# Performance work log

Hardware: AMD Instinct MI355X
Metric: run time of the kernel (lower is better)

## Reference

```python
import jax, jax.numpy as jnp
import numpy as np

B, C_IN, C_OUT, A, H, W = 32, 256, 512, 256, 64, 64


def setup_inputs() -> dict:
    key = jax.random.key(0)
    ks = jax.random.split(key, 8)
    s = 0.02
    return {
        "x": jax.random.normal(ks[0], (B, C_IN, H, W), dtype=jnp.float32),
        "g": jax.random.normal(ks[1], (B, C_OUT), dtype=jnp.float32),
        "Wg": jax.random.normal(ks[2], (A, C_OUT), dtype=jnp.float32) * s,
        "bg": jnp.full((A,), 0.1, dtype=jnp.float32),
        "Wx": jax.random.normal(ks[3], (A, C_IN), dtype=jnp.float32) * s,
        "bx": jnp.full((A,), 0.1, dtype=jnp.float32),
        "Wf": jax.random.normal(ks[4], (1, A), dtype=jnp.float32) * s,
        "bf": jnp.full((1,), 0.1, dtype=jnp.float32),
    }


def reference(x, g, Wg, bg, Wx, bx, Wf, bf):
    b, c, h, w = x.shape
    gg = g @ Wg.T + bg                                  # [B, A]
    xf = x.reshape(b, c, h * w)                          # [B, C, HW]
    # Linear_x applied per spatial position (batched instead of python loop)
    nx = jnp.einsum('bcn,ac->bna', xf, Wx) + bx          # [B, HW, A]
    nx = jax.nn.relu(gg[:, None, :] + nx)                # [B, HW, A]
    att = jnp.einsum('bna,a->bn', nx, Wf[0]) + bf[0]     # [B, HW]
    # min-subtract, sum-divide normalization
    att = att - jnp.min(att, axis=1, keepdims=True)
    att = att / jnp.sum(att, axis=1, keepdims=True)
    out = jnp.einsum('bcn,bn->bc', xf, att)              # weighted pooling [B, C]
    return out, att.reshape(b, h, w)
```

## Files before the change

kernel.cpp:

```cpp
#include <hip/hip_runtime.h>
#include <stdint.h>

#define B_   32
#define CIN  256
#define COUT 512
#define A_   256
#define HW_  4096
#define NT   64
#define TILES 8

typedef short  short8  __attribute__((ext_vector_type(8)));
typedef float  float4_ __attribute__((ext_vector_type(4)));

typedef const __attribute__((address_space(1))) unsigned int glb_uint;
typedef __attribute__((address_space(3))) unsigned int lds_uint;

__device__ __forceinline__ unsigned f2bf(float f) {
    unsigned u = __float_as_uint(f);
    u += 0x7FFFu + ((u >> 16) & 1u);
    return u >> 16;
}
__device__ __forceinline__ float bf2f(unsigned h) {
    return __uint_as_float(h << 16);
}

__device__ __forceinline__ void bar_lds() {
    __builtin_amdgcn_sched_barrier(0);
    asm volatile("s_waitcnt lgkmcnt(0)" ::: "memory");
    __builtin_amdgcn_s_barrier();
    __builtin_amdgcn_sched_barrier(0);
}

__global__ __launch_bounds__(256) void prep_kernel(
    const float* __restrict__ g, const float* __restrict__ Wg,
    const float* __restrict__ bg, const float* __restrict__ Wx,
    const float* __restrict__ bx,
    uint4* __restrict__ WxR, float* __restrict__ ggbx,
    float* __restrict__ P, float* __restrict__ T)
{
    int t = threadIdx.x;
    if (blockIdx.x >= 32) {
        int e = (blockIdx.x - 32) * 256 + t;
        int lane = e & 63, ai = (e >> 6) & 3, kk = (e >> 8) & 7, w = e >> 11;
        int a  = w * 64 + ai * 16 + (lane & 15);
        int kb = kk * 32 + (lane >> 4) * 8;
        const float4* s = (const float4*)(Wx + (size_t)a * 256 + kb);
        float4 u0 = s[0], u1 = s[1];
        uint4 pk;
        pk.x = f2bf(u0.x) | (f2bf(u0.y) << 16);
        pk.y = f2bf(u0.z) | (f2bf(u0.w) << 16);
        pk.z = f2bf(u1.x) | (f2bf(u1.y) << 16);
        pk.w = f2bf(u1.z) | (f2bf(u1.w) << 16);
        WxR[e] = pk;
        return;
    }
    int b = blockIdx.x;
    int i = b * 256 + t;
    P[i] = 0.f; T[i] = 0.f;

    __shared__ float gl[COUT];
    gl[t]       = g[b * COUT + t];
    gl[t + 256] = g[b * COUT + 256 + t];
    __syncthreads();

    float acc0 = bg[t] + bx[t], acc1 = 0.f;
    const float4* wr = (const float4*)(Wg + (size_t)t * COUT);
    #pragma unroll 8
    for (int co = 0; co < COUT / 4; co += 2) {
        float4 wv0 = wr[co],     gv0 = *(const float4*)&gl[co * 4];
        float4 wv1 = wr[co + 1], gv1 = *(const float4*)&gl[co * 4 + 4];
        acc0 += wv0.x * gv0.x + wv0.y * gv0.y + wv0.z * gv0.z + wv0.w * gv0.w;
        acc1 += wv1.x * gv1.x + wv1.y * gv1.y + wv1.z * gv1.z + wv1.w * gv1.w;
    }
    ggbx[b * 256 + t] = acc0 + acc1;
}

__global__ __launch_bounds__(512)
__attribute__((amdgpu_waves_per_eu(2, 2)))
void attn_main(
    const float* __restrict__ x, const char* __restrict__ WxR,
    const float* __restrict__ ggbx, const float* __restrict__ Wf,
    const float* __restrict__ bfs,
    float* __restrict__ P, float* __restrict__ T, float* __restrict__ raw)
{
    __shared__ float        rawb[CIN * NT];
    __shared__ unsigned int xT[2][NT * 128];
    __shared__ float att_part[8][NT];
    __shared__ float raw_l[NT];

    int bid = blockIdx.x;
    int b = bid >> 3, tg = bid & 7;
    int t = threadIdx.x, w = t >> 6, lane = t & 63;
    int quad = lane >> 4, l15 = lane & 15;
    int st = (tg + b) & 7;

    const float* xb = x + (size_t)b * CIN * HW_ + tg * (TILES * NT);

    auto STAGE = [&](int tile) {
        const float* gb = xb + (size_t)(w * 32 + (lane >> 4)) * HW_
                             + tile * NT + (lane & 15) * 4;
        #pragma unroll
        for (int j = 0; j < 8; j++) {
            __builtin_amdgcn_global_load_lds(
                (glb_uint*)(gb + (size_t)j * 4 * HW_),
                (lds_uint*)&rawb[(w * 8 + j) * 256], 16, 0, 0);
        }
    };

    short8 bfp[16];
    {
        const char* wsl = WxR + (w >> 1) * 32768 + (w & 1) * 2048 + lane * 16;
        #pragma unroll
        for (int kk = 0; kk < 8; kk++) {
            bfp[kk * 2]     = *(const short8*)(wsl + kk * 4096);
            bfp[kk * 2 + 1] = *(const short8*)(wsl + kk * 4096 + 1024);
        }
    }

    float4_ ga4[2], wf4[2];
    #pragma unroll
    for (int ai = 0; ai < 2; ai++) {
        int a0 = w * 32 + ai * 16 + quad * 4;
        ga4[ai] = *(const float4_*)&ggbx[b * 256 + a0];
        wf4[ai] = *(const float4_*)&Wf[a0];
    }

    float pp[4] = {0.f, 0.f, 0.f, 0.f};
    float tt[4] = {0.f, 0.f, 0.f, 0.f};
    int qpt   = (t & 63) >> 1;
    int half  = (t & 1) * 8;
    int nbase = w * 8;

    STAGE(st);

    #pragma unroll 1
    for (int ii = 0; ii < TILES; ii++) {
        int it = (ii + st) & 7;
        unsigned int* xc = xT[ii & 1];

        __syncthreads();

        {
            int n = lane;
            #pragma unroll
            for (int p = 0; p < 4; p++) {
                int q = w * 4 + p;
                const float* rb = &rawb[(q * 8) * 64 + n];
                uint4 pk;
                pk.x = f2bf(rb[0])   | (f2bf(rb[64])  << 16);
                pk.y = f2bf(rb[128]) | (f2bf(rb[192]) << 16);
                pk.z = f2bf(rb[256]) | (f2bf(rb[320]) << 16);
                pk.w = f2bf(rb[384]) | (f2bf(rb[448]) << 16);
                *(uint4*)&xc[n * 128 + ((q ^ (n & 31)) << 2)] = pk;
            }
        }
        __syncthreads();

        if (ii < TILES - 1)
            STAGE((ii + 1 + st) & 7);

        const unsigned int* xl = xc;
        float4_ acc[4][2];
        #pragma unroll
        for (int mi = 0; mi < 4; mi++) {
            acc[mi][0] = (float4_){0.f, 0.f, 0.f, 0.f};
            acc[mi][1] = (float4_){0.f, 0.f, 0.f, 0.f};
        }
        short8 afA[4], afB[4];
        auto LDA = [&](short8* af, int k0) {
            int qk = (k0 >> 3) + quad;
            #pragma unroll
            for (int mi = 0; mi < 4; mi++) {
                int n = mi * 16 + l15;
                af[mi] = *(const short8*)&xl[n * 128 + ((qk ^ (n & 31)) << 2)];
            }
        };
        auto MM = [&](short8* af, int ks) {
            #pragma unroll
            for (int mi = 0; mi < 4; mi++) {
                acc[mi][0] = __builtin_amdgcn_mfma_f32_16x16x32_bf16(
                    bfp[ks * 2],     af[mi], acc[mi][0], 0, 0, 0);
                acc[mi][1] = __builtin_amdgcn_mfma_f32_16x16x32_bf16(
                    bfp[ks * 2 + 1], af[mi], acc[mi][1], 0, 0, 0);
            }
        };

        LDA(afA, 0);   LDA(afB, 32);
        MM(afA, 0);    LDA(afA, 64);
        MM(afB, 1);    LDA(afB, 96);
        MM(afA, 2);    LDA(afA, 128);
        MM(afB, 3);    LDA(afB, 160);
        MM(afA, 4);    LDA(afA, 192);
        MM(afB, 5);    LDA(afB, 224);
        MM(afA, 6);
        MM(afB, 7);

        #pragma unroll
        for (int mi = 0; mi < 4; mi++) {
            float p = 0.f;
            #pragma unroll
            for (int ai = 0; ai < 2; ai++) {
                #pragma unroll
                for (int r = 0; r < 4; r++) {
                    float vv = fmaxf(acc[mi][ai][r] + ga4[ai][r], 0.f);
                    p = fmaf(vv, wf4[ai][r], p);
                }
            }
            p += __shfl_xor(p, 16, 64);
            p += __shfl_xor(p, 32, 64);
            if (quad == 0) att_part[w][mi * 16 + l15] = p;
        }
        bar_lds();

        if (t < NT) {
            float rv = att_part[0][t] + att_part[1][t] + att_part[2][t] + att_part[3][t]
                     + att_part[4][t] + att_part[5][t] + att_part[6][t] + att_part[7][t]
                     + bfs[0];
            raw[b * HW_ + (tg * TILES + it) * NT + t] = rv;
            raw_l[t] = rv;
        }
        bar_lds();

        #pragma unroll
        for (int i = 0; i < 8; i++) {
            int n = nbase + i;
            uint2 u = *(const uint2*)((const char*)xl + n * 512 + ((qpt ^ (n & 31)) << 4) + half);
            float rv = raw_l[n];
            float x0 = bf2f(u.x & 0xFFFFu), x1 = bf2f(u.x >> 16);
            float x2 = bf2f(u.y & 0xFFFFu), x3 = bf2f(u.y >> 16);
            pp[0] = fmaf(x0, rv, pp[0]); tt[0] += x0;
            pp[1] = fmaf(x1, rv, pp[1]); tt[1] += x1;
            pp[2] = fmaf(x2, rv, pp[2]); tt[2] += x2;
            pp[3] = fmaf(x3, rv, pp[3]); tt[3] += x3;
        }
    }

    {
        float* red = (float*)xT;
        float4_* pr = (float4_*)(red + w * 512);
        float4_* tr = (float4_*)(red + w * 512 + 256);
        pr[lane] = (float4_){pp[0], pp[1], pp[2], pp[3]};
        tr[lane] = (float4_){tt[0], tt[1], tt[2], tt[3]};
        __syncthreads();
        int sel = t >> 8, cc = t & 255;
        float s = 0.f;
        #pragma unroll
        for (int g = 0; g < 8; g++)
            s += red[g * 512 + sel * 256 + cc];
        atomicAdd((sel ? T : P) + b * 256 + cc, s);
    }
}

__global__ __launch_bounds__(256) void finalize_kernel(
    const float* __restrict__ raw, const float* __restrict__ P,
    const float* __restrict__ T, float* __restrict__ out)
{
    int b = blockIdx.x, t = threadIdx.x;
    const float* r = raw + (size_t)b * HW_;
    float v[16];
    float mn = 3.4e38f, sm = 0.f;
    #pragma unroll
    for (int i = 0; i < 16; i++) {
        v[i] = r[t + 256 * i];
        mn = fminf(mn, v[i]);
        sm += v[i];
    }
    #pragma unroll
    for (int off = 1; off < 64; off <<= 1) {
        mn = fminf(mn, __shfl_xor(mn, off, 64));
        sm += __shfl_xor(sm, off, 64);
    }
    __shared__ float smn[4], ssm[4];
    int w = t >> 6;
    if ((t & 63) == 0) { smn[w] = mn; ssm[w] = sm; }
    __syncthreads();
    mn = fminf(fminf(smn[0], smn[1]), fminf(smn[2], smn[3]));
    sm = (ssm[0] + ssm[1]) + (ssm[2] + ssm[3]);
    float S = sm - 4096.f * mn;
    float inv = 1.f / S;

    float* att = out + B_ * CIN + (size_t)b * HW_;
    #pragma unroll
    for (int i = 0; i < 16; i++) att[t + 256 * i] = (v[i] - mn) * inv;

    int ic = b * 256 + t;
    out[ic] = (P[ic] - mn * T[ic]) * inv;
}

extern "C" void kernel_launch(void* const* d_in, const int* in_sizes, int n_in,
                              void* d_out, int out_size, void* d_ws, size_t ws_size,
                              hipStream_t stream)
{
    const float* x   = (const float*)d_in[0];
    const float* g   = (const float*)d_in[1];
    const float* Wg  = (const float*)d_in[2];
    const float* bg  = (const float*)d_in[3];
    const float* Wx  = (const float*)d_in[4];
    const float* bx  = (const float*)d_in[5];
    const float* Wf  = (const float*)d_in[6];
    const float* bf  = (const float*)d_in[7];
    float* out = (float*)d_out;

    char* wsb = (char*)d_ws;
    uint4* WxR  = (uint4*)wsb;
    float* ggbx = (float*)(wsb + 131072);
    float* P    = ggbx + 8192;
    float* T    = P + 8192;
    float* raw  = T + 8192;

    prep_kernel<<<64, 256, 0, stream>>>(g, Wg, bg, Wx, bx, WxR, ggbx, P, T);
    attn_main<<<256, 512, 0, stream>>>(x, (const char*)WxR, ggbx, Wf, bf, P, T, raw);
    finalize_kernel<<<32, 256, 0, stream>>>(raw, P, T, out);
}
```

Baseline: 232.1 us.

## Split fp32-to-bf16 transpose of x into a separate pre-pass kernel

Adds an xprep kernel that reads x, converts it to bf16 and writes a pre-swizzled, transposed per-block layout into workspace. attn_main then streams that layout straight into LDS, dropping the large fp32 staging buffer, the in-loop conversion and one barrier per tile. This frees LDS and removes conversion work from the main loop, but costs an extra kernel launch plus a full global write and re-read of x as bf16 (about half the fp32 size).

```diff
diff --git a/kernel.cpp b/kernel.cpp
--- a/kernel.cpp
+++ b/kernel.cpp
@@ -75,15 +75,60 @@
     ggbx[b * 256 + t] = acc0 + acc1;
 }
 
+__global__ __launch_bounds__(512) void xprep_kernel(
+    const float* __restrict__ x, char* __restrict__ xTg)
+{
+    __shared__ float rawb[2][32 * 512];
+    int bid = blockIdx.x;
+    int b = bid >> 3, tg = bid & 7;
+    int t = threadIdx.x, w = t >> 6, lane = t & 63;
+
+    const float* xw_ = x + (size_t)b * CIN * HW_ + (size_t)(w * 4) * HW_
+                         + tg * 512 + lane * 4;
+    auto XSTAGE = [&](int cg, int bufi) {
+        const float* gb = xw_ + (size_t)(cg * 32) * HW_;
+        #pragma unroll
+        for (int j = 0; j < 4; j++) {
+            #pragma unroll
+            for (int h = 0; h < 2; h++) {
+                __builtin_amdgcn_global_load_lds(
+                    (glb_uint*)(gb + (size_t)j * HW_ + h * 256),
+                    (lds_uint*)&rawb[bufi][(w * 4 + j) * 512 + h * 256],
+                    16, 0, 0);
+            }
+        }
+    };
+
+    int tau = t >> 6, tn = t & 63, m = tn & 31;
+    char* outb = xTg + (size_t)bid * 262144 + tau * 32768 + tn * 512;
+
+    XSTAGE(0, 0);
+    #pragma unroll 1
+    for (int cg = 0; cg < 8; cg++) {
+        __syncthreads();
+        if (cg < 7) XSTAGE(cg + 1, (cg + 1) & 1);
+        const float* rb = &rawb[cg & 1][t];
+        char* ob = outb + ((cg ^ (m >> 2)) << 6);
+        #pragma unroll
+        for (int qq = 0; qq < 4; qq++) {
+            unsigned wd0 = f2bf(rb[(qq * 8 + 0) * 512]) | (f2bf(rb[(qq * 8 + 1) * 512]) << 16);
+            unsigned wd1 = f2bf(rb[(qq * 8 + 2) * 512]) | (f2bf(rb[(qq * 8 + 3) * 512]) << 16);
+            unsigned wd2 = f2bf(rb[(qq * 8 + 4) * 512]) | (f2bf(rb[(qq * 8 + 5) * 512]) << 16);
+            unsigned wd3 = f2bf(rb[(qq * 8 + 6) * 512]) | (f2bf(rb[(qq * 8 + 7) * 512]) << 16);
+            uint4 pk; pk.x = wd0; pk.y = wd1; pk.z = wd2; pk.w = wd3;
+            *(uint4*)(ob + ((qq ^ (m & 3)) << 4)) = pk;
+        }
+    }
+}
+
 __global__ __launch_bounds__(512)
 __attribute__((amdgpu_waves_per_eu(2, 2)))
 void attn_main(
-    const float* __restrict__ x, const char* __restrict__ WxR,
+    const char* __restrict__ xTg, const char* __restrict__ WxR,
     const float* __restrict__ ggbx, const float* __restrict__ Wf,
     const float* __restrict__ bfs,
     float* __restrict__ P, float* __restrict__ T, float* __restrict__ raw)
 {
-    __shared__ float        rawb[CIN * NT];
     __shared__ unsigned int xT[2][NT * 128];
     __shared__ float att_part[8][NT];
     __shared__ float raw_l[NT];
@@ -94,16 +139,15 @@
     int quad = lane >> 4, l15 = lane & 15;
     int st = (tg + b) & 7;
 
-    const float* xb = x + (size_t)b * CIN * HW_ + tg * (TILES * NT);
-
-    auto STAGE = [&](int tile) {
-        const float* gb = xb + (size_t)(w * 32 + (lane >> 4)) * HW_
-                             + tile * NT + (lane & 15) * 4;
-        #pragma unroll
-        for (int j = 0; j < 8; j++) {
+    const char* xg = xTg + (size_t)bid * 262144;
+
+    auto STAGE = [&](int tile, int bufi) {
+        const char* gb = xg + tile * 32768 + w * 4096 + lane * 16;
+        #pragma unroll
+        for (int j = 0; j < 4; j++) {
             __builtin_amdgcn_global_load_lds(
-                (glb_uint*)(gb + (size_t)j * 4 * HW_),
-                (lds_uint*)&rawb[(w * 8 + j) * 256], 16, 0, 0);
+                (glb_uint*)(gb + j * 1024),
+                (lds_uint*)&xT[bufi][w * 1024 + j * 256], 16, 0, 0);
         }
     };
 
@@ -131,35 +175,19 @@
     int half  = (t & 1) * 8;
     int nbase = w * 8;
 
-    STAGE(st);
+    STAGE(st, 0);
 
     #pragma unroll 1
     for (int ii = 0; ii < TILES; ii++) {
         int it = (ii + st) & 7;
-        unsigned int* xc = xT[ii & 1];
 
         __syncthreads();
 
-        {
-            int n = lane;
-            #pragma unroll
-            for (int p = 0; p < 4; p++) {
-                int q = w * 4 + p;
-                const float* rb = &rawb[(q * 8) * 64 + n];
-                uint4 pk;
-                pk.x = f2bf(rb[0])   | (f2bf(rb[64])  << 16);
-                pk.y = f2bf(rb[128]) | (f2bf(rb[192]) << 16);
-                pk.z = f2bf(rb[256]) | (f2bf(rb[320]) << 16);
-                pk.w = f2bf(rb[384]) | (f2bf(rb[448]) << 16);
-                *(uint4*)&xc[n * 128 + ((q ^ (n & 31)) << 2)] = pk;
-            }
-        }
-        __syncthreads();
-
         if (ii < TILES - 1)
-            STAGE((ii + 1 + st) & 7);
-
-        const unsigned int* xl = xc;
+            STAGE((ii + 1 + st) & 7, (ii + 1) & 1);
+
+        const unsigned int* xl = xT[ii & 1];
+
         float4_ acc[4][2];
         #pragma unroll
         for (int mi = 0; mi < 4; mi++) {
@@ -236,6 +264,7 @@
     }
 
     {
+        __syncthreads();
         float* red = (float*)xT;
         float4_* pr = (float4_*)(red + w * 512);
         float4_* tr = (float4_*)(red + w * 512 + 256);
@@ -307,8 +336,10 @@
     float* P    = ggbx + 8192;
     float* T    = P + 8192;
     float* raw  = T + 8192;
+    char* xTg   = wsb + (1 << 20);
 
     prep_kernel<<<64, 256, 0, stream>>>(g, Wg, bg, Wx, bx, WxR, ggbx, P, T);
-    attn_main<<<256, 512, 0, stream>>>(x, (const char*)WxR, ggbx, Wf, bf, P, T, raw);
+    xprep_kernel<<<256, 512, 0, stream>>>(x, xTg);
+    attn_main<<<256, 512, 0, stream>>>(xTg, (const char*)WxR, ggbx, Wf, bf, P, T, raw);
     finalize_kernel<<<32, 256, 0, stream>>>(raw, P, T, out);
 }
```

Result: slower. 275.6 us (+18.7%).
